# Optimization experiments

Hardware: AMD Instinct MI355X
Metric: run time of the kernel (lower is better)

Reference implementation:

```python
import jax, jax.numpy as jnp
import numpy as np

B, T, IN, H, L, C = 64, 2048, 64, 128, 2, 8


def setup_inputs() -> dict:
    key = jax.random.key(0)
    ks = jax.random.split(key, 11)
    s = 1.0 / np.sqrt(H)  # torch nn.RNN default init scale
    return {
        "x": jax.random.normal(ks[0], (B, T, IN), dtype=jnp.float32),
        "W_ih0": jax.random.uniform(ks[1], (H, IN), jnp.float32, -s, s),
        "W_hh0": jax.random.uniform(ks[2], (H, H), jnp.float32, -s, s),
        "b_ih0": jax.random.uniform(ks[3], (H,), jnp.float32, -s, s),
        "b_hh0": jax.random.uniform(ks[4], (H,), jnp.float32, -s, s),
        "W_ih1": jax.random.uniform(ks[5], (H, H), jnp.float32, -s, s),
        "W_hh1": jax.random.uniform(ks[6], (H, H), jnp.float32, -s, s),
        "b_ih1": jax.random.uniform(ks[7], (H,), jnp.float32, -s, s),
        "b_hh1": jax.random.uniform(ks[8], (H,), jnp.float32, -s, s),
        "W_fc": jax.random.uniform(ks[9], (C, H), jnp.float32, -s, s),
        "b_fc": jax.random.uniform(ks[10], (C,), jnp.float32, -s, s),
    }


def _rnn_layer(x, W_ih, W_hh, b_ih, b_hh):
    # x: (B, T, D_in) -> (B, T, H); h0 = zeros (matches torch h0)
    # Precompute the input projection as one big GEMM outside the scan.
    x_proj = jnp.einsum('btd,hd->bth', x, W_ih) + b_ih + b_hh  # (B,T,H)
    x_proj_t = jnp.swapaxes(x_proj, 0, 1)  # (T,B,H)
    h0 = jnp.zeros((x.shape[0], W_hh.shape[0]), dtype=x.dtype)

    def step(h, xp):
        h_new = jnp.tanh(xp + h @ W_hh.T)
        return h_new, h_new

    _, hs = jax.lax.scan(step, h0, x_proj_t)  # (T,B,H)
    return jnp.swapaxes(hs, 0, 1)  # (B,T,H)


def reference(x, W_ih0, W_hh0, b_ih0, b_hh0, W_ih1, W_hh1, b_ih1, b_hh1, W_fc, b_fc):
    h1 = _rnn_layer(x, W_ih0, W_hh0, b_ih0, b_hh0)   # layer 0
    h2 = _rnn_layer(h1, W_ih1, W_hh1, b_ih1, b_hh1)  # layer 1
    logits = jnp.einsum('bth,ch->btc', h2, W_fc) + b_fc  # (B,T,C)
    return logits
```

## Files before the change

### kernel.cpp

```cpp
#include <hip/hip_runtime.h>

#define B_ 64
#define T_ 2048
#define IN_ 64
#define H_ 128
#define C_ 8

typedef _Float16 f16x2 __attribute__((ext_vector_type(2)));

__device__ __forceinline__ f16x2 pkw(float a, float b) {
  return __builtin_bit_cast(f16x2, __builtin_amdgcn_cvt_pkrtz(a, b));
}
__device__ __forceinline__ f16x2 pk_rne(float a, float b) {
  f16x2 r; r.x = (_Float16)a; r.y = (_Float16)b; return r;
}
__device__ __forceinline__ f16x2 as_h2(int v) { return __builtin_bit_cast(f16x2, v); }

__device__ __forceinline__ float dot2(f16x2 a, f16x2 b, float c) {
#if __has_builtin(__builtin_amdgcn_fdot2)
  return __builtin_amdgcn_fdot2(a, b, c, false);
#else
  float r;
  asm("v_dot2_f32_f16 %0, %1, %2, %3" : "=v"(r) : "v"(a), "v"(b), "v"(c));
  return r;
#endif
}

__device__ __forceinline__ float tanh_fast(float x) {
  float e = __builtin_amdgcn_exp2f(x * 2.8853900817779268f);
  return 1.0f - 2.0f * __builtin_amdgcn_rcpf(e + 1.0f);
}

template <int CTRL>
__device__ __forceinline__ float dpp_add(float v) {
  return v + __int_as_float(__builtin_amdgcn_update_dpp(
                 0, __float_as_int(v), CTRL, 0xF, 0xF, true));
}
__device__ __forceinline__ float red4(float v) {
  return dpp_add<0x4E>(dpp_add<0xB1>(v));
}
__device__ __forceinline__ float red8(float v) {
  return dpp_add<0x141>(dpp_add<0x4E>(dpp_add<0xB1>(v)));
}

__device__ __forceinline__ void block_sync_lds() {
  asm volatile("s_waitcnt lgkmcnt(0)" ::: "memory");
  __builtin_amdgcn_s_barrier();
  asm volatile("" ::: "memory");
}

#define DOT8(A, Q, W, BASE)            \
  A = dot2(as_h2(Q.x), W[BASE+0], A);  \
  A = dot2(as_h2(Q.y), W[BASE+1], A);  \
  A = dot2(as_h2(Q.z), W[BASE+2], A);  \
  A = dot2(as_h2(Q.w), W[BASE+3], A);

__global__ __launch_bounds__(256) void k_xproj(
    const float* __restrict__ x, const float* __restrict__ Wih0,
    const float* __restrict__ bih0, const float* __restrict__ bhh0,
    _Float16* __restrict__ xp) {
  __shared__ __align__(16) _Float16 xs[4][2][IN_];
  const int wave = threadIdx.x >> 6, lane = threadIdx.x & 63;
  const int gw = blockIdx.x * 4 + wave;
  const int ROWS = 32;
  const size_t r0 = (size_t)gw * ROWS;

  f16x2 wA[32], wB[32];
  const float2* W2 = (const float2*)Wih0;
#pragma unroll
  for (int p = 0; p < 32; ++p) {
    float2 a = W2[(lane * 2) * 32 + p];
    float2 b = W2[(lane * 2 + 1) * 32 + p];
    wA[p] = pkw(a.x, a.y); wB[p] = pkw(b.x, b.y);
  }
  const float ba = bih0[lane * 2] + bhh0[lane * 2];
  const float bb = bih0[lane * 2 + 1] + bhh0[lane * 2 + 1];

  xs[wave][0][lane] = (_Float16)x[r0 * IN_ + lane];
  float xn = x[(r0 + 1) * IN_ + lane];
  for (int rr = 0; rr < ROWS; ++rr) {
    const int buf = rr & 1;
    if (rr + 1 < ROWS) xs[wave][buf ^ 1][lane] = (_Float16)xn;
    if (rr + 2 < ROWS) xn = x[(r0 + rr + 2) * IN_ + lane];
    asm volatile("s_waitcnt lgkmcnt(0)" ::: "memory");
    const int4* xv = (const int4*)xs[wave][buf];
    int4 q0 = xv[0], q1 = xv[1], q2 = xv[2], q3 = xv[3];
    int4 q4 = xv[4], q5 = xv[5], q6 = xv[6], q7 = xv[7];
    float a0 = 0.f, a1 = 0.f, c0 = 0.f, c1 = 0.f;
    DOT8(a0, q0, wA, 0)  DOT8(c0, q0, wB, 0)
    DOT8(a1, q1, wA, 4)  DOT8(c1, q1, wB, 4)
    DOT8(a0, q2, wA, 8)  DOT8(c0, q2, wB, 8)
    DOT8(a1, q3, wA, 12) DOT8(c1, q3, wB, 12)
    DOT8(a0, q4, wA, 16) DOT8(c0, q4, wB, 16)
    DOT8(a1, q5, wA, 20) DOT8(c1, q5, wB, 20)
    DOT8(a0, q6, wA, 24) DOT8(c0, q6, wB, 24)
    DOT8(a1, q7, wA, 28) DOT8(c1, q7, wB, 28)
    *(f16x2*)&xp[(r0 + rr) * H_ + lane * 2] = pk_rne(a0 + a1 + ba, c0 + c1 + bb);
  }
}


#define L0PH(PP, XA, RB, WPB)                                          \
  {                                                                    \
    block_sync_lds();                                                  \
    const int p_ = (PP);                                               \
    if (p_ < T_) {                                                     \
      const float fx = (float)XA.x, fy = (float)XA.y;                  \
      int4 q0 = hp[(RB) + kq4 + 0], q1 = hp[(RB) + kq4 + 1];           \
      int4 q2 = hp[(RB) + kq4 + 2], q3 = hp[(RB) + kq4 + 3];           \
      float a0 = 0.f, a1 = 0.f, c0 = 0.f, c1 = 0.f;                    \
      DOT8(a0, q0, wA, 0)  DOT8(c0, q0, wB, 0)                         \
      DOT8(a1, q1, wA, 4)  DOT8(c1, q1, wB, 4)                         \
      DOT8(a0, q2, wA, 8)  DOT8(c0, q2, wB, 8)                         \
      DOT8(a1, q3, wA, 12) DOT8(c1, q3, wB, 12)                        \
      float t0 = tanh_fast(red4(a0 + a1) + fx);                        \
      float t1 = tanh_fast(red4(c0 + c1) + fy);                        \
      if (kq == 0) {                                                   \
        wp[(WPB) + jx] = pk_rne(t0, t1);                               \
        const int pp = p_ + 4;                                         \
        if (pp < T_) XA = xp2[xpb + (size_t)pp * 64 + jx];             \
      }                                                                \
    }                                                                  \
  }

#define L1PH(PP, RH2, WPB, RH1)                                        \
  {                                                                    \
    block_sync_lds();                                                  \
    const int p_ = (PP);                                               \
    if (p_ >= 2 && p_ < T_ + 2) {                                      \
      int4 h0 = hp[(RH2) + kg2], h1v = hp[(RH2) + kg2 + 1];            \
      float a = pi0, c = pi1;                                          \
      DOT8(a, h0, whA, 0) DOT8(a, h1v, whA, 4)                         \
      DOT8(c, h0, whB, 0) DOT8(c, h1v, whB, 4)                         \
      float t0 = tanh_fast(red8(a) + bA);                              \
      float t1 = tanh_fast(red8(c) + bB);                              \
      if (kg == 0) wp[(WPB) + jy] = pk_rne(t0, t1);                    \
    }                                                                  \
    if (p_ <= T_) {                                                    \
      int4 g0 = hp[(RH1) + kg2], g1 = hp[(RH1) + kg2 + 1];             \
      float x0 = 0.f, x1 = 0.f;                                        \
      DOT8(x0, g0, wiA, 0) DOT8(x0, g1, wiA, 4)                        \
      DOT8(x1, g0, wiB, 0) DOT8(x1, g1, wiB, 4)                        \
      pi0 = x0; pi1 = x1;                                              \
    }                                                                  \
  }

#define FCPH(PP, RB)                                                   \
  {                                                                    \
    block_sync_lds();                                                  \
    const int p_ = (PP);                                               \
    if (p_ >= 3 && p_ < T_ + 3) {                                      \
      int4 h0 = hp[(RB) + kg2], h1v = hp[(RB) + kg2 + 1];              \
      float a = 0.f;                                                   \
      DOT8(a, h0, wf, 0) DOT8(a, h1v, wf, 4)                           \
      float r = red8(a);                                               \
      if (k8 == 0) outb[(size_t)(p_ - 3) * C_ + cc] = r + bv;          \
    }                                                                  \
  }

__global__ __launch_bounds__(832) void k_rnn(
    const _Float16* __restrict__ xp0,
    const float* __restrict__ Whh0,
    const float* __restrict__ Wih1,
    const float* __restrict__ Whh1,
    const float* __restrict__ bih1,
    const float* __restrict__ bhh1,
    const float* __restrict__ Wfc,
    const float* __restrict__ bfc,
    float* __restrict__ out) {
  __shared__ __align__(16) _Float16 hlds[4][H_];

  const int tid  = threadIdx.x;
  const int wave = tid >> 6;
  const int lane = tid & 63;
  const int b    = blockIdx.x;

  if (tid < 256) ((int*)hlds)[tid] = 0;
  const int4* hp = (const int4*)hlds;
  f16x2*      wp = (f16x2*)hlds;
  block_sync_lds();

  if (wave < 4) {
    const int jj = lane >> 2, kq = lane & 3;
    const int kq4 = kq * 4;
    const int j0 = wave * 32 + jj * 2;
    const int jx = wave * 16 + jj;
    f16x2 wA[16], wB[16];
    const float2* W2 = (const float2*)Whh0;
#pragma unroll
    for (int m = 0; m < 4; ++m)
#pragma unroll
      for (int e = 0; e < 4; ++e) {
        float2 a = W2[j0 * 64 + kq * 16 + m * 4 + e];
        float2 bt = W2[(j0 + 1) * 64 + kq * 16 + m * 4 + e];
        wA[m * 4 + e] = pkw(a.x, a.y);
        wB[m * 4 + e] = pkw(bt.x, bt.y);
      }
    const size_t xpb = (size_t)b * T_ * 64;
    const f16x2* xp2 = (const f16x2*)xp0;
    f16x2 XA0 = {0,0}, XA1 = {0,0}, XA2 = {0,0}, XA3 = {0,0};
    if (kq == 0) {
      XA0 = xp2[xpb + 0 * 64 + jx]; XA1 = xp2[xpb + 1 * 64 + jx];
      XA2 = xp2[xpb + 2 * 64 + jx]; XA3 = xp2[xpb + 3 * 64 + jx];
    }
    for (int p0 = 0; p0 < T_ + 4; p0 += 4) {
      L0PH(p0 + 0, XA0, 16, 0)
      L0PH(p0 + 1, XA1, 0, 64)
      L0PH(p0 + 2, XA2, 16, 0)
      L0PH(p0 + 3, XA3, 0, 64)
    }
  } else if (wave < 12) {
    const int u = wave - 4;
    const int jj = lane >> 3, kg = lane & 7;
    const int kg2 = kg * 2;
    const int j0 = u * 16 + jj * 2;
    const int jy = u * 8 + jj;
    f16x2 whA[8], whB[8], wiA[8], wiB[8];
    const float2* Wh2 = (const float2*)Whh1;
    const float2* Wi2 = (const float2*)Wih1;
#pragma unroll
    for (int n = 0; n < 8; ++n) {
      float2 a = Wi2[j0 * 64 + kg * 8 + n];        wiA[n] = pkw(a.x, a.y);
      float2 bq = Wi2[(j0 + 1) * 64 + kg * 8 + n]; wiB[n] = pkw(bq.x, bq.y);
      float2 cq = Wh2[j0 * 64 + kg * 8 + n];       whA[n] = pkw(cq.x, cq.y);
      float2 dq = Wh2[(j0 + 1) * 64 + kg * 8 + n]; whB[n] = pkw(dq.x, dq.y);
    }
    const float bA = bih1[j0] + bhh1[j0];
    const float bB = bih1[j0 + 1] + bhh1[j0 + 1];
    float pi0 = 0.f, pi1 = 0.f;
    for (int p0 = 0; p0 < T_ + 4; p0 += 2) {
      L1PH(p0 + 0, 48, 128, 16)
      L1PH(p0 + 1, 32, 192, 0)
    }
  } else {
    const int cc = lane >> 3, k8 = lane & 7;
    const int kg2 = k8 * 2;
    f16x2 wf[8];
    const float2* W2 = (const float2*)Wfc;
#pragma unroll
    for (int n = 0; n < 8; ++n) {
      float2 a = W2[cc * 64 + k8 * 8 + n];
      wf[n] = pkw(a.x, a.y);
    }
    const float bv = bfc[cc];
    float* outb = out + (size_t)b * T_ * C_;
    for (int p0 = 0; p0 < T_ + 4; p0 += 2) {
      FCPH(p0 + 0, 48)
      FCPH(p0 + 1, 32)
    }
  }
}

extern "C" void kernel_launch(void* const* d_in, const int* in_sizes, int n_in,
                              void* d_out, int out_size, void* d_ws, size_t ws_size,
                              hipStream_t stream) {
  const float* x    = (const float*)d_in[0];
  const float* Wih0 = (const float*)d_in[1];
  const float* Whh0 = (const float*)d_in[2];
  const float* bih0 = (const float*)d_in[3];
  const float* bhh0 = (const float*)d_in[4];
  const float* Wih1 = (const float*)d_in[5];
  const float* Whh1 = (const float*)d_in[6];
  const float* bih1 = (const float*)d_in[7];
  const float* bhh1 = (const float*)d_in[8];
  const float* Wfc  = (const float*)d_in[9];
  const float* bfc  = (const float*)d_in[10];
  float* outp = (float*)d_out;
  _Float16* xp0 = (_Float16*)d_ws;

  k_xproj<<<1024, 256, 0, stream>>>(x, Wih0, bih0, bhh0, xp0);
  k_rnn<<<64, 832, 0, stream>>>(xp0, Whh0, Wih1, Whh1, bih1, bhh1, Wfc, bfc, outp);
}
```

Before: 1.108 ms.

## Fold FC wave into layer-1 wave, peel loop guards, raise layer-0 priority

```diff
diff --git a/kernel.cpp b/kernel.cpp
--- a/kernel.cpp
+++ b/kernel.cpp
@@ -62,7 +62,7 @@
   __shared__ __align__(16) _Float16 xs[4][2][IN_];
   const int wave = threadIdx.x >> 6, lane = threadIdx.x & 63;
   const int gw = blockIdx.x * 4 + wave;
-  const int ROWS = 32;
+  const int ROWS = 16;
   const size_t r0 = (size_t)gw * ROWS;
 
   f16x2 wA[32], wB[32];
@@ -100,11 +100,11 @@
 }
 
 
-#define L0PH(PP, XA, RB, WPB)                                          \
+#define L0PH(PP, XA, RB, WPB, G)                                       \
   {                                                                    \
     block_sync_lds();                                                  \
     const int p_ = (PP);                                               \
-    if (p_ < T_) {                                                     \
+    if (!(G) || (p_ < T_)) {                                           \
       const float fx = (float)XA.x, fy = (float)XA.y;                  \
       int4 q0 = hp[(RB) + kq4 + 0], q1 = hp[(RB) + kq4 + 1];           \
       int4 q2 = hp[(RB) + kq4 + 2], q3 = hp[(RB) + kq4 + 3];           \
@@ -115,19 +115,18 @@
       DOT8(a1, q3, wA, 12) DOT8(c1, q3, wB, 12)                        \
       float t0 = tanh_fast(red4(a0 + a1) + fx);                        \
       float t1 = tanh_fast(red4(c0 + c1) + fy);                        \
-      if (kq == 0) {                                                   \
-        wp[(WPB) + jx] = pk_rne(t0, t1);                               \
-        const int pp = p_ + 4;                                         \
-        if (pp < T_) XA = xp2[xpb + (size_t)pp * 64 + jx];             \
-      }                                                                \
-    }                                                                  \
-  }
-
-#define L1PH(PP, RH2, WPB, RH1)                                        \
+      if (kq == 0) wp[(WPB) + jx] = pk_rne(t0, t1);                    \
+    }                                                                  \
+    if (!(G) || (p_ + 4 < T_)) {                                       \
+      XA = xp2[xpb + (size_t)(p_ + 4) * 64 + jx];                      \
+    }                                                                  \
+  }
+
+#define L1PH(PP, RH2, WPB, RH1, G)                                     \
   {                                                                    \
     block_sync_lds();                                                  \
     const int p_ = (PP);                                               \
-    if (p_ >= 2 && p_ < T_ + 2) {                                      \
+    if (!(G) || (p_ >= 2 && p_ < T_ + 2)) {                            \
       int4 h0 = hp[(RH2) + kg2], h1v = hp[(RH2) + kg2 + 1];            \
       float a = pi0, c = pi1;                                          \
       DOT8(a, h0, whA, 0) DOT8(a, h1v, whA, 4)                         \
@@ -136,7 +135,14 @@
       float t1 = tanh_fast(red8(c) + bB);                              \
       if (kg == 0) wp[(WPB) + jy] = pk_rne(t0, t1);                    \
     }                                                                  \
-    if (p_ <= T_) {                                                    \
+    if (fcw && (!(G) || (p_ >= 3 && p_ < T_ + 3))) {                   \
+      int4 f0 = hp[(RH2) + kg2], f1 = hp[(RH2) + kg2 + 1];             \
+      float fa = 0.f;                                                  \
+      DOT8(fa, f0, wf, 0) DOT8(fa, f1, wf, 4)                          \
+      float fr = red8(fa);                                             \
+      if (kg == 0) outb[(size_t)(p_ - 3) * C_ + jj] = fr + bv;         \
+    }                                                                  \
+    if (!(G) || (p_ <= T_)) {                                          \
       int4 g0 = hp[(RH1) + kg2], g1 = hp[(RH1) + kg2 + 1];             \
       float x0 = 0.f, x1 = 0.f;                                        \
       DOT8(x0, g0, wiA, 0) DOT8(x0, g1, wiA, 4)                        \
@@ -145,20 +151,7 @@
     }                                                                  \
   }
 
-#define FCPH(PP, RB)                                                   \
-  {                                                                    \
-    block_sync_lds();                                                  \
-    const int p_ = (PP);                                               \
-    if (p_ >= 3 && p_ < T_ + 3) {                                      \
-      int4 h0 = hp[(RB) + kg2], h1v = hp[(RB) + kg2 + 1];              \
-      float a = 0.f;                                                   \
-      DOT8(a, h0, wf, 0) DOT8(a, h1v, wf, 4)                           \
-      float r = red8(a);                                               \
-      if (k8 == 0) outb[(size_t)(p_ - 3) * C_ + cc] = r + bv;          \
-    }                                                                  \
-  }
-
-__global__ __launch_bounds__(832) void k_rnn(
+__global__ __launch_bounds__(768) void k_rnn(
     const _Float16* __restrict__ xp0,
     const float* __restrict__ Whh0,
     const float* __restrict__ Wih1,
@@ -198,24 +191,31 @@
       }
     const size_t xpb = (size_t)b * T_ * 64;
     const f16x2* xp2 = (const f16x2*)xp0;
-    f16x2 XA0 = {0,0}, XA1 = {0,0}, XA2 = {0,0}, XA3 = {0,0};
-    if (kq == 0) {
-      XA0 = xp2[xpb + 0 * 64 + jx]; XA1 = xp2[xpb + 1 * 64 + jx];
-      XA2 = xp2[xpb + 2 * 64 + jx]; XA3 = xp2[xpb + 3 * 64 + jx];
-    }
-    for (int p0 = 0; p0 < T_ + 4; p0 += 4) {
-      L0PH(p0 + 0, XA0, 16, 0)
-      L0PH(p0 + 1, XA1, 0, 64)
-      L0PH(p0 + 2, XA2, 16, 0)
-      L0PH(p0 + 3, XA3, 0, 64)
-    }
-  } else if (wave < 12) {
+    f16x2 XA0 = xp2[xpb + 0 * 64 + jx], XA1 = xp2[xpb + 1 * 64 + jx];
+    f16x2 XA2 = xp2[xpb + 2 * 64 + jx], XA3 = xp2[xpb + 3 * 64 + jx];
+    __builtin_amdgcn_s_setprio(1);
+    L0PH(0, XA0, 16, 0, 1) L0PH(1, XA1, 0, 64, 1)
+    L0PH(2, XA2, 16, 0, 1) L0PH(3, XA3, 0, 64, 1)
+    for (int p0 = 4; p0 < 2040; p0 += 4) {
+      L0PH(p0 + 0, XA0, 16, 0, 0)
+      L0PH(p0 + 1, XA1, 0, 64, 0)
+      L0PH(p0 + 2, XA2, 16, 0, 0)
+      L0PH(p0 + 3, XA3, 0, 64, 0)
+    }
+    for (int p0 = 2040; p0 < 2052; p0 += 4) {
+      L0PH(p0 + 0, XA0, 16, 0, 1)
+      L0PH(p0 + 1, XA1, 0, 64, 1)
+      L0PH(p0 + 2, XA2, 16, 0, 1)
+      L0PH(p0 + 3, XA3, 0, 64, 1)
+    }
+  } else {
     const int u = wave - 4;
     const int jj = lane >> 3, kg = lane & 7;
     const int kg2 = kg * 2;
     const int j0 = u * 16 + jj * 2;
     const int jy = u * 8 + jj;
-    f16x2 whA[8], whB[8], wiA[8], wiB[8];
+    const bool fcw = (u == 0);
+    f16x2 whA[8], whB[8], wiA[8], wiB[8], wf[8];
     const float2* Wh2 = (const float2*)Whh1;
     const float2* Wi2 = (const float2*)Wih1;
 #pragma unroll
@@ -225,28 +225,29 @@
       float2 cq = Wh2[j0 * 64 + kg * 8 + n];       whA[n] = pkw(cq.x, cq.y);
       float2 dq = Wh2[(j0 + 1) * 64 + kg * 8 + n]; whB[n] = pkw(dq.x, dq.y);
     }
+    float bv = 0.f;
+    if (fcw) {
+      const float2* Wf2 = (const float2*)Wfc;
+#pragma unroll
+      for (int n = 0; n < 8; ++n) {
+        float2 a = Wf2[jj * 64 + kg * 8 + n];
+        wf[n] = pkw(a.x, a.y);
+      }
+      bv = bfc[jj];
+    }
     const float bA = bih1[j0] + bhh1[j0];
     const float bB = bih1[j0 + 1] + bhh1[j0 + 1];
+    float* outb = out + (size_t)b * T_ * C_;
     float pi0 = 0.f, pi1 = 0.f;
-    for (int p0 = 0; p0 < T_ + 4; p0 += 2) {
-      L1PH(p0 + 0, 48, 128, 16)
-      L1PH(p0 + 1, 32, 192, 0)
-    }
-  } else {
-    const int cc = lane >> 3, k8 = lane & 7;
-    const int kg2 = k8 * 2;
-    f16x2 wf[8];
-    const float2* W2 = (const float2*)Wfc;
-#pragma unroll
-    for (int n = 0; n < 8; ++n) {
-      float2 a = W2[cc * 64 + k8 * 8 + n];
-      wf[n] = pkw(a.x, a.y);
-    }
-    const float bv = bfc[cc];
-    float* outb = out + (size_t)b * T_ * C_;
-    for (int p0 = 0; p0 < T_ + 4; p0 += 2) {
-      FCPH(p0 + 0, 48)
-      FCPH(p0 + 1, 32)
+    L1PH(0, 48, 128, 16, 1) L1PH(1, 32, 192, 0, 1)
+    L1PH(2, 48, 128, 16, 1) L1PH(3, 32, 192, 0, 1)
+    for (int p0 = 4; p0 < 2040; p0 += 2) {
+      L1PH(p0 + 0, 48, 128, 16, 0)
+      L1PH(p0 + 1, 32, 192, 0, 0)
+    }
+    for (int p0 = 2040; p0 < 2052; p0 += 2) {
+      L1PH(p0 + 0, 48, 128, 16, 1)
+      L1PH(p0 + 1, 32, 192, 0, 1)
     }
   }
 }
@@ -268,6 +269,6 @@
   float* outp = (float*)d_out;
   _Float16* xp0 = (_Float16*)d_ws;
 
-  k_xproj<<<1024, 256, 0, stream>>>(x, Wih0, bih0, bhh0, xp0);
-  k_rnn<<<64, 832, 0, stream>>>(xp0, Whh0, Wih1, Whh1, bih1, bhh1, Wfc, bfc, outp);
-}
+  k_xproj<<<2048, 256, 0, stream>>>(x, Wih0, bih0, bhh0, xp0);
+  k_rnn<<<64, 768, 0, stream>>>(xp0, Whh0, Wih1, Whh1, bih1, bhh1, Wfc, bfc, outp);
+}
```

Result: faster. 1.012 ms (-8.6%).
